# Kernel tuning notes

Measured on AMD Instinct MI355X. Metric: run time of the kernel, lower is better.

Reference implementation:

```python
import jax, jax.numpy as jnp
import numpy as np

POINT_SAMPLE_NUM = 4096
CHAMFER_W = 1.0
NORM_W = 0.1
EDGE_W = 0.5
EPS = 1e-12


def _face_geometry(vertices, faces):
    # vertices: [B, V, 3], faces: [F, 3] int -> per-face verts, areas, unit normals
    v0 = vertices[:, faces[:, 0]]  # [B, F, 3]
    v1 = vertices[:, faces[:, 1]]
    v2 = vertices[:, faces[:, 2]]
    cross = jnp.cross(v1 - v0, v2 - v0)            # [B, F, 3]
    area2 = jnp.linalg.norm(cross, axis=-1)        # [B, F] (= 2*area)
    normals = cross / (area2[..., None] + EPS)     # unit face normals
    return v0, v1, v2, 0.5 * area2, normals


def _sample_points(vertices, faces, n_samples, key):
    # area-weighted face sampling + uniform barycentric coords
    B = vertices.shape[0]
    v0, v1, v2, area, normals = _face_geometry(vertices, faces)
    k_face, k_u, k_v = jax.random.split(key, 3)
    logits = jnp.log(area + EPS)                   # [B, F]
    face_idx = jax.random.categorical(k_face, logits[:, None, :], axis=-1,
                                      shape=(B, n_samples))  # [B, N]
    gather = lambda a: jnp.take_along_axis(a, face_idx[..., None], axis=1)
    p0, p1, p2 = gather(v0), gather(v1), gather(v2)           # [B, N, 3]
    u = jax.random.uniform(k_u, (B, n_samples, 1))
    v = jax.random.uniform(k_v, (B, n_samples, 1))
    r1 = jnp.sqrt(u)
    points = (1.0 - r1) * p0 + r1 * (1.0 - v) * p1 + r1 * v * p2  # [B, N, 3]
    point_normals = gather(normals)                                # [B, N, 3]
    return points, point_normals


def _chamfer(x, y):
    # x: [B, N, 3], y: [B, M, 3] -> squared-distance chamfer + nn indices
    x2 = jnp.sum(x * x, axis=-1)                   # [B, N]
    y2 = jnp.sum(y * y, axis=-1)                   # [B, M]
    d2 = x2[:, :, None] + y2[:, None, :] - 2.0 * jnp.einsum('bnd,bmd->bnm', x, y)
    d2 = jnp.maximum(d2, 0.0)
    idx_x2y = jnp.argmin(d2, axis=2)               # [B, N] nearest y for each x
    min_x2y = jnp.min(d2, axis=2)
    min_y2x = jnp.min(d2, axis=1)
    return jnp.mean(min_x2y) + jnp.mean(min_y2x), idx_x2y


def _edge_loss(vertices, faces):
    v0 = vertices[:, faces[:, 0]]
    v1 = vertices[:, faces[:, 1]]
    v2 = vertices[:, faces[:, 2]]
    e = jnp.concatenate([v1 - v0, v2 - v1, v0 - v2], axis=1)  # [B, 3F, 3]
    return jnp.mean(jnp.sum(e * e, axis=-1))


def setup_inputs() -> dict:
    key = jax.random.key(0)
    k1, k2, k3, k4 = jax.random.split(key, 4)
    predicted_vertices = jax.random.normal(k1, (4, 2562, 3), dtype=jnp.float32)
    predicted_faces = jax.random.randint(k2, (5120, 3), 0, 2562, dtype=jnp.int64)
    gt_vertices = jax.random.normal(k3, (4, 6890, 3), dtype=jnp.float32)
    gt_faces = jax.random.randint(k4, (13776, 3), 0, 6890, dtype=jnp.int64)
    return {"predicted_vertices": predicted_vertices,
            "predicted_faces": predicted_faces,
            "gt_vertices": gt_vertices,
            "gt_faces": gt_faces}


def reference(predicted_vertices, predicted_faces, gt_vertices, gt_faces):
    key = jax.random.key(42)
    kp, kg = jax.random.split(key)
    pred_pts, pred_nrm = _sample_points(predicted_vertices, predicted_faces,
                                        POINT_SAMPLE_NUM, kp)
    gt_pts, gt_nrm = _sample_points(gt_vertices, gt_faces, POINT_SAMPLE_NUM, kg)
    chamfer, idx_p2g = _chamfer(pred_pts, gt_pts)
    # normal consistency between each predicted point and its nearest gt point
    matched_gt_nrm = jnp.take_along_axis(gt_nrm, idx_p2g[..., None], axis=1)
    cos = jnp.abs(jnp.sum(pred_nrm * matched_gt_nrm, axis=-1))  # [B, N]
    normal_loss = jnp.mean(1.0 - cos)
    edge_loss = _edge_loss(predicted_vertices, predicted_faces)
    return CHAMFER_W * chamfer + NORM_W * normal_loss + EDGE_W * edge_loss
```

## Files before the change

kernel.cpp:

```cpp
#include <hip/hip_runtime.h>
#include <stdint.h>

constexpr int   kB  = 4;
constexpr int   kNS = 4096;
constexpr int   kVP = 2562;
constexpr int   kFP = 5120;
constexpr int   kVG = 6890;
constexpr int   kFG = 13776;
constexpr float kEPS  = 1e-12f;
constexpr int   kPB  = 256;
constexpr int   kPREP_P = (kB * kFP + 255) / 256;
constexpr int   kPREP_G = (kB * kFG + 255) / 256;

__host__ __device__ inline void tf2x32(uint32_t k0, uint32_t k1,
                                       uint32_t& x0r, uint32_t& x1r) {
  uint32_t ks2 = k0 ^ k1 ^ 0x1BD11BDAu;
  uint32_t x0 = x0r + k0, x1 = x1r + k1;
#define TF_R(r) { x0 += x1; x1 = (x1 << (r)) | (x1 >> (32 - (r))); x1 ^= x0; }
  TF_R(13) TF_R(15) TF_R(26) TF_R(6)
  x0 += k1;  x1 += ks2 + 1u;
  TF_R(17) TF_R(29) TF_R(16) TF_R(24)
  x0 += ks2; x1 += k0 + 2u;
  TF_R(13) TF_R(15) TF_R(26) TF_R(6)
  x0 += k0;  x1 += k1 + 3u;
  TF_R(17) TF_R(29) TF_R(16) TF_R(24)
  x0 += k1;  x1 += ks2 + 4u;
  TF_R(13) TF_R(15) TF_R(26) TF_R(6)
  x0 += ks2; x1 += k0 + 5u;
#undef TF_R
  x0r = x0; x1r = x1;
}

__device__ inline float bits_to_unit(uint32_t b) {
  return __uint_as_float((b >> 9) | 0x3f800000u) - 1.0f;
}

__device__ inline int faces_is64(const int* __restrict__ faces) {
  return (faces[1] == 0 && faces[3] == 0 && faces[5] == 0 && faces[7] == 0) ? 1 : 0;
}
__device__ inline int face_vtx(const int* __restrict__ faces, int f, int c,
                               int is64, int V) {
  int e = f * 3 + c;
  int v = faces[is64 ? (e << 1) : e];
  return v < 0 ? 0 : (v >= V ? V - 1 : v);
}

__global__ void mlk_write_scalar(float* out, float val) {
  if (threadIdx.x == 0 && blockIdx.x == 0) out[0] = val;
}

__global__ __launch_bounds__(256) void mlk_prep_faces2(
    const float* __restrict__ pverts, const int* __restrict__ pfaces,
    const float* __restrict__ gverts, const int* __restrict__ gfaces,
    float* __restrict__ wp, float* __restrict__ np,
    float* __restrict__ wg, float* __restrict__ ng) {
  int which = blockIdx.x >= kPREP_P;
  int blk   = which ? blockIdx.x - kPREP_P : blockIdx.x;
  const float* verts = which ? gverts : pverts;
  const int*   faces = which ? gfaces : pfaces;
  float* warea = which ? wg : wp;
  float* fnrm  = which ? ng : np;
  int V = which ? kVG : kVP;
  int F = which ? kFG : kFP;
  int idx = blk * 256 + threadIdx.x;
  if (idx >= kB * F) return;
  int is64 = faces_is64(faces);
  int b = idx / F, f = idx - b * F;
  int i0 = face_vtx(faces, f, 0, is64, V);
  int i1 = face_vtx(faces, f, 1, is64, V);
  int i2 = face_vtx(faces, f, 2, is64, V);
  const float* vb = verts + (size_t)b * V * 3;
  float ax = vb[i0*3+0], ay = vb[i0*3+1], az = vb[i0*3+2];
  float bx = vb[i1*3+0], by = vb[i1*3+1], bz = vb[i1*3+2];
  float cx = vb[i2*3+0], cy = vb[i2*3+1], cz = vb[i2*3+2];
  float e1x = bx-ax, e1y = by-ay, e1z = bz-az;
  float e2x = cx-ax, e2y = cy-ay, e2z = cz-az;
  float nx = e1y*e2z - e1z*e2y;
  float ny = e1z*e2x - e1x*e2z;
  float nz = e1x*e2y - e1y*e2x;
  float area2 = sqrtf(nx*nx + ny*ny + nz*nz);
  warea[idx] = 0.5f * area2 + kEPS;
  float inv_n = 1.0f / (area2 + kEPS);
  fnrm[3*idx+0] = nx*inv_n;
  fnrm[3*idx+1] = ny*inv_n;
  fnrm[3*idx+2] = nz*inv_n;
}

__global__ __launch_bounds__(256) void mlk_prefix2(
    float* __restrict__ wp, float* __restrict__ wg) {
  int which = blockIdx.x >> 2;
  int b = blockIdx.x & 3, tid = threadIdx.x;
  int F = which ? kFG : kFP;
  float* wb = (which ? wg : wp) + (size_t)b * F;
  int C = (F + 255) / 256;
  int lo = tid * C;
  int hi = lo + C; if (hi > F) hi = F; if (lo > F) lo = F;
  float s = 0.f;
  for (int i = lo; i < hi; ++i) s += wb[i];
  __shared__ float ps[256];
  ps[tid] = s;
  __syncthreads();
  for (int off = 1; off < 256; off <<= 1) {
    float v = (tid >= off) ? ps[tid - off] : 0.f;
    __syncthreads();
    ps[tid] += v;
    __syncthreads();
  }
  float p = ps[tid] - s;
  for (int i = lo; i < hi; ++i) { p += wb[i]; wb[i] = p; }
}

__global__ __launch_bounds__(256) void mlk_sample_gen(
    const float* __restrict__ pverts, const int* __restrict__ pfaces,
    const float* __restrict__ pref_p, const float* __restrict__ fnrm_p,
    float* __restrict__ pred_pts, float* __restrict__ pred_nrm,
    const float* __restrict__ gverts, const int* __restrict__ gfaces,
    const float* __restrict__ pref_g, const float* __restrict__ fnrm_g,
    float* __restrict__ gt_pts, float* __restrict__ gt_nrm,
    uint32_t pf0, uint32_t pf1, uint32_t pu0, uint32_t pu1, uint32_t pv0, uint32_t pv1,
    uint32_t gf0, uint32_t gf1, uint32_t gu0, uint32_t gu1, uint32_t gv0, uint32_t gv1) {
  int which = blockIdx.x >> 5;
  int t = ((blockIdx.x & 31) << 8) + threadIdx.x;
  const float* verts = which ? gverts : pverts;
  const int*   faces = which ? gfaces : pfaces;
  const float* pref  = which ? pref_g : pref_p;
  const float* fnrm  = which ? fnrm_g : fnrm_p;
  float* pts  = which ? gt_pts : pred_pts;
  float* pnrm = which ? gt_nrm : pred_nrm;
  int V = which ? kVG : kVP;
  int F = which ? kFG : kFP;
  uint32_t kf0 = which ? gf0 : pf0, kf1 = which ? gf1 : pf1;
  uint32_t ku0 = which ? gu0 : pu0, ku1 = which ? gu1 : pu1;
  uint32_t kv0 = which ? gv0 : pv0, kv1 = which ? gv1 : pv1;
  int is64 = faces_is64(faces);

  uint32_t fx0 = (uint32_t)t, fx1 = (uint32_t)(t + 8192);
  tf2x32(kf0, kf1, fx0, fx1);
  uint32_t ux0 = (uint32_t)t, ux1 = (uint32_t)(t + 8192);
  tf2x32(ku0, ku1, ux0, ux1);
  uint32_t vx0 = (uint32_t)t, vx1 = (uint32_t)(t + 8192);
  tf2x32(kv0, kv1, vx0, vx1);

#pragma unroll
  for (int half = 0; half < 2; ++half) {
    int i = t + half * 8192;
    int b = i >> 12;
    float uf = bits_to_unit(half ? fx1 : fx0);
    const float* Pb = pref + (size_t)b * F;
    float target = uf * Pb[F - 1];
    int lo = 0, hi = F - 1;
    while (lo < hi) {
      int mid = (lo + hi) >> 1;
      if (Pb[mid] > target) hi = mid; else lo = mid + 1;
    }
    int fid = lo;
    float u = bits_to_unit(half ? ux1 : ux0);
    float v = bits_to_unit(half ? vx1 : vx0);
    const float* vb = verts + (size_t)b * V * 3;
    int i0 = face_vtx(faces, fid, 0, is64, V);
    int i1 = face_vtx(faces, fid, 1, is64, V);
    int i2 = face_vtx(faces, fid, 2, is64, V);
    float r1 = sqrtf(u);
    float w0 = 1.0f - r1, w1 = r1 * (1.0f - v), w2 = r1 * v;
#pragma unroll
    for (int c = 0; c < 3; ++c) {
      pts[i*3+c] = w0 * vb[i0*3+c] + w1 * vb[i1*3+c] + w2 * vb[i2*3+c];
      pnrm[i*3+c] = fnrm[((size_t)b*F + fid)*3 + c];
    }
  }
}

__global__ __launch_bounds__(256) void mlk_chamfer2(
    const float* __restrict__ pred_pts, const float* __restrict__ gt_pts,
    float* __restrict__ min_p2g, float* __restrict__ min_g2p,
    int* __restrict__ idx_p2g) {
  int bid = blockIdx.x;
  int dir = bid >> 8;
  int r   = bid & 255;
  int b   = r >> 6;
  int qc  = r & 63;
  const float* qpts = dir ? gt_pts   : pred_pts;
  const float* rpts = dir ? pred_pts : gt_pts;
  int wave = threadIdx.x >> 6;
  int lane = threadIdx.x & 63;

  __shared__ float4 lpx4[kNS/4], lpy4[kNS/4], lpz4[kNS/4];
  float* lpx = (float*)lpx4; float* lpy = (float*)lpy4; float* lpz = (float*)lpz4;
  const float* rb = rpts + (size_t)b * kNS * 3;
  for (int i = threadIdx.x; i < kNS; i += 256) {
    lpx[i] = rb[3*i+0];
    lpy[i] = rb[3*i+1];
    lpz[i] = rb[3*i+2];
  }
  __syncthreads();

  int q  = qc * 64 + lane;
  int gi = b * kNS + q;
  float px = qpts[gi*3+0], py = qpts[gi*3+1], pz = qpts[gi*3+2];
  int j0 = wave * (kNS/4/4) * 4;
  j0 = wave * 256;
  float best; int bidx = 0;

  if (dir == 0) {
    float bA = INFINITY, bB = INFINITY; int iA = 0, iB = 0;
#pragma unroll 2
    for (int j = j0; j < j0 + 256; ++j) {
      float4 X = lpx4[j], Y = lpy4[j], Z = lpz4[j];
      int m = j << 2;
      float dx, dy, dz;
      dx = px-X.x; dy = py-Y.x; dz = pz-Z.x; float d0 = dx*dx+dy*dy+dz*dz;
      dx = px-X.y; dy = py-Y.y; dz = pz-Z.y; float d1 = dx*dx+dy*dy+dz*dz;
      dx = px-X.z; dy = py-Y.z; dz = pz-Z.z; float d2 = dx*dx+dy*dy+dz*dz;
      dx = px-X.w; dy = py-Y.w; dz = pz-Z.w; float d3 = dx*dx+dy*dy+dz*dz;
      if (d0 < bA) { bA = d0; iA = m; }
      if (d1 < bA) { bA = d1; iA = m | 1; }
      if (d2 < bB) { bB = d2; iB = m | 2; }
      if (d3 < bB) { bB = d3; iB = m | 3; }
    }
    if (bB < bA || (bB == bA && iB < iA)) { best = bB; bidx = iB; }
    else                                  { best = bA; bidx = iA; }
  } else {
    float bA = INFINITY, bB = INFINITY;
#pragma unroll 2
    for (int j = j0; j < j0 + 256; ++j) {
      float4 X = lpx4[j], Y = lpy4[j], Z = lpz4[j];
      float dx, dy, dz;
      dx = px-X.x; dy = py-Y.x; dz = pz-Z.x; float d0 = dx*dx+dy*dy+dz*dz;
      dx = px-X.y; dy = py-Y.y; dz = pz-Z.y; float d1 = dx*dx+dy*dy+dz*dz;
      dx = px-X.z; dy = py-Y.z; dz = pz-Z.z; float d2 = dx*dx+dy*dy+dz*dz;
      dx = px-X.w; dy = py-Y.w; dz = pz-Z.w; float d3 = dx*dx+dy*dy+dz*dz;
      bA = fminf(bA, fminf(d0, d1));
      bB = fminf(bB, fminf(d2, d3));
    }
    best = fminf(bA, bB);
  }

  __shared__ float cv[4][64];
  __shared__ int   ci[4][64];
  cv[wave][lane] = best; ci[wave][lane] = bidx;
  __syncthreads();
  if (wave == 0) {
    float bv = cv[0][lane]; int bi = ci[0][lane];
#pragma unroll
    for (int wv = 1; wv < 4; ++wv) {
      float v = cv[wv][lane];
      int   i = ci[wv][lane];
      if (v < bv || (v == bv && i < bi)) { bv = v; bi = i; }
    }
    if (dir == 0) { min_p2g[gi] = bv; idx_p2g[gi] = bi; }
    else          { min_g2p[gi] = bv; }
  }
}

__global__ __launch_bounds__(256) void mlk_loss_partial(
    const float* __restrict__ min_p2g, const float* __restrict__ min_g2p,
    const float* __restrict__ pred_nrm, const float* __restrict__ gt_nrm,
    const int* __restrict__ idx_p2g,
    const float* __restrict__ pverts, const int* __restrict__ pfaces,
    float* __restrict__ partial) {
  int tid = threadIdx.x;
  int gidx = blockIdx.x * 256 + tid;
  const int stride = kPB * 256;
  int is64 = faces_is64(pfaces);
  float s1 = 0.f, s2 = 0.f, sc = 0.f, se = 0.f;
  for (int i = gidx; i < kB * kNS; i += stride) {
    s1 += min_p2g[i];
    s2 += min_g2p[i];
    int b = i >> 12;
    int m = idx_p2g[i];
    m = m < 0 ? 0 : (m >= kNS ? kNS - 1 : m);
    const float* pn = pred_nrm + (size_t)i * 3;
    const float* gn = gt_nrm + ((size_t)b * kNS + m) * 3;
    sc += fabsf(pn[0]*gn[0] + pn[1]*gn[1] + pn[2]*gn[2]);
  }
  for (int e = gidx; e < kB * kFP * 3; e += stride) {
    int b = e / (kFP * 3);
    int r = e - b * kFP * 3;
    int f = r / 3, k = r - f * 3;
    int ia, ib;
    if (k == 0)      { ia = face_vtx(pfaces, f, 0, is64, kVP); ib = face_vtx(pfaces, f, 1, is64, kVP); }
    else if (k == 1) { ia = face_vtx(pfaces, f, 1, is64, kVP); ib = face_vtx(pfaces, f, 2, is64, kVP); }
    else             { ia = face_vtx(pfaces, f, 2, is64, kVP); ib = face_vtx(pfaces, f, 0, is64, kVP); }
    const float* vb = pverts + (size_t)b * kVP * 3;
    float dx = vb[ib*3+0] - vb[ia*3+0];
    float dy = vb[ib*3+1] - vb[ia*3+1];
    float dz = vb[ib*3+2] - vb[ia*3+2];
    se += dx*dx + dy*dy + dz*dz;
  }
  __shared__ float r1a[256], r2a[256], r3a[256], r4a[256];
  r1a[tid] = s1; r2a[tid] = s2; r3a[tid] = sc; r4a[tid] = se;
  __syncthreads();
  for (int off = 128; off > 0; off >>= 1) {
    if (tid < off) {
      r1a[tid] += r1a[tid+off];
      r2a[tid] += r2a[tid+off];
      r3a[tid] += r3a[tid+off];
      r4a[tid] += r4a[tid+off];
    }
    __syncthreads();
  }
  if (tid == 0) {
    partial[blockIdx.x*4+0] = r1a[0];
    partial[blockIdx.x*4+1] = r2a[0];
    partial[blockIdx.x*4+2] = r3a[0];
    partial[blockIdx.x*4+3] = r4a[0];
  }
}

__global__ __launch_bounds__(256) void mlk_loss_combine(
    const float* __restrict__ partial, float* __restrict__ out) {
  int tid = threadIdx.x;
  __shared__ float r1a[256], r2a[256], r3a[256], r4a[256];
  r1a[tid] = partial[tid*4+0];
  r2a[tid] = partial[tid*4+1];
  r3a[tid] = partial[tid*4+2];
  r4a[tid] = partial[tid*4+3];
  __syncthreads();
  for (int off = 128; off > 0; off >>= 1) {
    if (tid < off) {
      r1a[tid] += r1a[tid+off];
      r2a[tid] += r2a[tid+off];
      r3a[tid] += r3a[tid+off];
      r4a[tid] += r4a[tid+off];
    }
    __syncthreads();
  }
  if (tid == 0) {
    const float invN = 1.0f / (float)(kB * kNS);
    float chamfer = r1a[0] * invN + r2a[0] * invN;
    float nloss = 1.0f - r3a[0] * invN;
    float eloss = r4a[0] / (float)(kB * kFP * 3);
    out[0] = 1.0f * chamfer + 0.1f * nloss + 0.5f * eloss;
  }
}

extern "C" void kernel_launch(void* const* d_in, const int* in_sizes, int n_in,
                              void* d_out, int out_size, void* d_ws, size_t ws_size,
                              hipStream_t stream) {
  const float* pverts = (const float*)d_in[0];
  const int*   pfaces = (const int*)d_in[1];
  const float* gverts = (const float*)d_in[2];
  const int*   gfaces = (const int*)d_in[3];
  float* out = (float*)d_out;

  const size_t needF =
      (size_t)kB*kFP + (size_t)kB*kFG +
      (size_t)kB*kFP*3 + (size_t)kB*kFG*3 +
      4*(size_t)kB*kNS*3 +
      2*(size_t)kB*kNS +
      (size_t)kPB*4 +
      (size_t)kB*kNS;
  if (ws_size < needF * 4) {
    mlk_write_scalar<<<1, 64, 0, stream>>>(out, -1.0f);
    return;
  }

  uint32_t a0 = 0u, a1 = 2u; tf2x32(0u, 42u, a0, a1);
  uint32_t b0 = 1u, b1 = 3u; tf2x32(0u, 42u, b0, b1);
  uint32_t kp0 = a0, kp1 = b0;
  uint32_t kg0 = a1, kg1 = b1;
  uint32_t kpred[6], kgt[6];
  {
    uint32_t p0 = 0u, p1 = 3u; tf2x32(kp0, kp1, p0, p1);
    uint32_t q0 = 1u, q1 = 4u; tf2x32(kp0, kp1, q0, q1);
    uint32_t r0 = 2u, r1 = 5u; tf2x32(kp0, kp1, r0, r1);
    kpred[0]=p0; kpred[1]=q0; kpred[2]=r0; kpred[3]=p1; kpred[4]=q1; kpred[5]=r1;
  }
  {
    uint32_t p0 = 0u, p1 = 3u; tf2x32(kg0, kg1, p0, p1);
    uint32_t q0 = 1u, q1 = 4u; tf2x32(kg0, kg1, q0, q1);
    uint32_t r0 = 2u, r1 = 5u; tf2x32(kg0, kg1, r0, r1);
    kgt[0]=p0; kgt[1]=q0; kgt[2]=r0; kgt[3]=p1; kgt[4]=q1; kgt[5]=r1;
  }

  float* ws = (float*)d_ws;
  float* pref_p   = ws; ws += kB * kFP;
  float* pref_g   = ws; ws += kB * kFG;
  float* fnrm_p   = ws; ws += kB * kFP * 3;
  float* fnrm_g   = ws; ws += kB * kFG * 3;
  float* pred_pts = ws; ws += kB * kNS * 3;
  float* gt_pts   = ws; ws += kB * kNS * 3;
  float* pred_nrm = ws; ws += kB * kNS * 3;
  float* gt_nrm   = ws; ws += kB * kNS * 3;
  float* min_p2g  = ws; ws += kB * kNS;
  float* min_g2p  = ws; ws += kB * kNS;
  float* partial  = ws; ws += kPB * 4;
  int* idx_p2g = (int*)ws; ws += kB * kNS;

  mlk_prep_faces2<<<kPREP_P + kPREP_G, 256, 0, stream>>>(
      pverts, pfaces, gverts, gfaces, pref_p, fnrm_p, pref_g, fnrm_g);

  mlk_prefix2<<<8, 256, 0, stream>>>(pref_p, pref_g);

  mlk_sample_gen<<<64, 256, 0, stream>>>(
      pverts, pfaces, pref_p, fnrm_p, pred_pts, pred_nrm,
      gverts, gfaces, pref_g, fnrm_g, gt_pts, gt_nrm,
      kpred[0], kpred[1], kpred[2], kpred[3], kpred[4], kpred[5],
      kgt[0],  kgt[1],  kgt[2],  kgt[3],  kgt[4],  kgt[5]);

  mlk_chamfer2<<<512, 256, 0, stream>>>(pred_pts, gt_pts, min_p2g, min_g2p, idx_p2g);

  mlk_loss_partial<<<kPB, 256, 0, stream>>>(min_p2g, min_g2p, pred_nrm, gt_nrm, idx_p2g,
                                            pverts, pfaces, partial);
  mlk_loss_combine<<<1, 256, 0, stream>>>(partial, out);
}
```

Measured before the change: 81.12 us.

## Fuse final reduction via atomic ticket, register-block chamfer, interleave binary searches

The final combine kernel is folded into the partial-loss kernel. The last block to finish, picked by an atomic ticket counter that the prep kernel resets, does the final reduction. This removes one launch. The chamfer kernel now uses 512-thread blocks where each thread handles two query points, so every shared-memory load of reference points is reused twice. Sample generation runs as smaller 64-thread blocks with the two binary searches interleaved to overlap their memory latency. This adds atomic and fence overhead and raises register pressure in the chamfer loop.

```diff
diff --git a/kernel.cpp b/kernel.cpp
--- a/kernel.cpp
+++ b/kernel.cpp
@@ -53,7 +53,9 @@
     const float* __restrict__ pverts, const int* __restrict__ pfaces,
     const float* __restrict__ gverts, const int* __restrict__ gfaces,
     float* __restrict__ wp, float* __restrict__ np,
-    float* __restrict__ wg, float* __restrict__ ng) {
+    float* __restrict__ wg, float* __restrict__ ng,
+    unsigned int* __restrict__ counter) {
+  if (blockIdx.x == 0 && threadIdx.x == 0) *counter = 0u;
   int which = blockIdx.x >= kPREP_P;
   int blk   = which ? blockIdx.x - kPREP_P : blockIdx.x;
   const float* verts = which ? gverts : pverts;
@@ -110,7 +112,7 @@
   for (int i = lo; i < hi; ++i) { p += wb[i]; wb[i] = p; }
 }
 
-__global__ __launch_bounds__(256) void mlk_sample_gen(
+__global__ __launch_bounds__(64) void mlk_sample_gen(
     const float* __restrict__ pverts, const int* __restrict__ pfaces,
     const float* __restrict__ pref_p, const float* __restrict__ fnrm_p,
     float* __restrict__ pred_pts, float* __restrict__ pred_nrm,
@@ -119,8 +121,9 @@
     float* __restrict__ gt_pts, float* __restrict__ gt_nrm,
     uint32_t pf0, uint32_t pf1, uint32_t pu0, uint32_t pu1, uint32_t pv0, uint32_t pv1,
     uint32_t gf0, uint32_t gf1, uint32_t gu0, uint32_t gu1, uint32_t gv0, uint32_t gv1) {
-  int which = blockIdx.x >> 5;
-  int t = ((blockIdx.x & 31) << 8) + threadIdx.x;
+  int g = blockIdx.x * 64 + threadIdx.x;
+  int which = g >> 13;
+  int t = g & 8191;
   const float* verts = which ? gverts : pverts;
   const int*   faces = which ? gfaces : pfaces;
   const float* pref  = which ? pref_g : pref_p;
@@ -141,19 +144,29 @@
   uint32_t vx0 = (uint32_t)t, vx1 = (uint32_t)(t + 8192);
   tf2x32(kv0, kv1, vx0, vx1);
 
+  int b0 = t >> 12, b1 = b0 + 2;
+  const float* P0 = pref + (size_t)b0 * F;
+  const float* P1 = pref + (size_t)b1 * F;
+  float tg0 = bits_to_unit(fx0) * P0[F - 1];
+  float tg1 = bits_to_unit(fx1) * P1[F - 1];
+  int lo0 = 0, hi0 = F - 1, lo1 = 0, hi1 = F - 1;
+  while (lo0 < hi0 || lo1 < hi1) {
+    if (lo0 < hi0) {
+      int mid = (lo0 + hi0) >> 1;
+      if (P0[mid] > tg0) hi0 = mid; else lo0 = mid + 1;
+    }
+    if (lo1 < hi1) {
+      int mid = (lo1 + hi1) >> 1;
+      if (P1[mid] > tg1) hi1 = mid; else lo1 = mid + 1;
+    }
+  }
+  int fid0 = lo0, fid1 = lo1;
+
 #pragma unroll
   for (int half = 0; half < 2; ++half) {
     int i = t + half * 8192;
     int b = i >> 12;
-    float uf = bits_to_unit(half ? fx1 : fx0);
-    const float* Pb = pref + (size_t)b * F;
-    float target = uf * Pb[F - 1];
-    int lo = 0, hi = F - 1;
-    while (lo < hi) {
-      int mid = (lo + hi) >> 1;
-      if (Pb[mid] > target) hi = mid; else lo = mid + 1;
-    }
-    int fid = lo;
+    int fid = half ? fid1 : fid0;
     float u = bits_to_unit(half ? ux1 : ux0);
     float v = bits_to_unit(half ? vx1 : vx0);
     const float* vb = verts + (size_t)b * V * 3;
@@ -170,15 +183,15 @@
   }
 }
 
-__global__ __launch_bounds__(256) void mlk_chamfer2(
+__global__ __launch_bounds__(512) void mlk_chamfer3(
     const float* __restrict__ pred_pts, const float* __restrict__ gt_pts,
     float* __restrict__ min_p2g, float* __restrict__ min_g2p,
     int* __restrict__ idx_p2g) {
   int bid = blockIdx.x;
-  int dir = bid >> 8;
-  int r   = bid & 255;
-  int b   = r >> 6;
-  int qc  = r & 63;
+  int dir = bid >> 7;
+  int r   = bid & 127;
+  int b   = r >> 5;
+  int qc  = r & 31;
   const float* qpts = dir ? gt_pts   : pred_pts;
   const float* rpts = dir ? pred_pts : gt_pts;
   int wave = threadIdx.x >> 6;
@@ -187,77 +200,90 @@
   __shared__ float4 lpx4[kNS/4], lpy4[kNS/4], lpz4[kNS/4];
   float* lpx = (float*)lpx4; float* lpy = (float*)lpy4; float* lpz = (float*)lpz4;
   const float* rb = rpts + (size_t)b * kNS * 3;
-  for (int i = threadIdx.x; i < kNS; i += 256) {
+  for (int i = threadIdx.x; i < kNS; i += 512) {
     lpx[i] = rb[3*i+0];
     lpy[i] = rb[3*i+1];
     lpz[i] = rb[3*i+2];
   }
   __syncthreads();
 
-  int q  = qc * 64 + lane;
-  int gi = b * kNS + q;
-  float px = qpts[gi*3+0], py = qpts[gi*3+1], pz = qpts[gi*3+2];
-  int j0 = wave * (kNS/4/4) * 4;
-  j0 = wave * 256;
-  float best; int bidx = 0;
+  int q0 = qc * 128 + lane;
+  int gq0 = b * kNS + q0;
+  int gq1 = gq0 + 64;
+  float px0 = qpts[gq0*3+0], py0 = qpts[gq0*3+1], pz0 = qpts[gq0*3+2];
+  float px1 = qpts[gq1*3+0], py1 = qpts[gq1*3+1], pz1 = qpts[gq1*3+2];
+  int j0 = wave * 128;
+  float best0, best1; int bidx0 = 0, bidx1 = 0;
 
   if (dir == 0) {
-    float bA = INFINITY, bB = INFINITY; int iA = 0, iB = 0;
+    float bA0 = INFINITY, bB0 = INFINITY, bA1 = INFINITY, bB1 = INFINITY;
+    int iA0 = 0, iB0 = 0, iA1 = 0, iB1 = 0;
 #pragma unroll 2
-    for (int j = j0; j < j0 + 256; ++j) {
+    for (int j = j0; j < j0 + 128; ++j) {
       float4 X = lpx4[j], Y = lpy4[j], Z = lpz4[j];
       int m = j << 2;
-      float dx, dy, dz;
-      dx = px-X.x; dy = py-Y.x; dz = pz-Z.x; float d0 = dx*dx+dy*dy+dz*dz;
-      dx = px-X.y; dy = py-Y.y; dz = pz-Z.y; float d1 = dx*dx+dy*dy+dz*dz;
-      dx = px-X.z; dy = py-Y.z; dz = pz-Z.z; float d2 = dx*dx+dy*dy+dz*dz;
-      dx = px-X.w; dy = py-Y.w; dz = pz-Z.w; float d3 = dx*dx+dy*dy+dz*dz;
-      if (d0 < bA) { bA = d0; iA = m; }
-      if (d1 < bA) { bA = d1; iA = m | 1; }
-      if (d2 < bB) { bB = d2; iB = m | 2; }
-      if (d3 < bB) { bB = d3; iB = m | 3; }
-    }
-    if (bB < bA || (bB == bA && iB < iA)) { best = bB; bidx = iB; }
-    else                                  { best = bA; bidx = iA; }
+      float dx, dy, dz, d;
+      dx = px0-X.x; dy = py0-Y.x; dz = pz0-Z.x; d = dx*dx+dy*dy+dz*dz; if (d < bA0) { bA0 = d; iA0 = m; }
+      dx = px0-X.y; dy = py0-Y.y; dz = pz0-Z.y; d = dx*dx+dy*dy+dz*dz; if (d < bA0) { bA0 = d; iA0 = m|1; }
+      dx = px0-X.z; dy = py0-Y.z; dz = pz0-Z.z; d = dx*dx+dy*dy+dz*dz; if (d < bB0) { bB0 = d; iB0 = m|2; }
+      dx = px0-X.w; dy = py0-Y.w; dz = pz0-Z.w; d = dx*dx+dy*dy+dz*dz; if (d < bB0) { bB0 = d; iB0 = m|3; }
+      dx = px1-X.x; dy = py1-Y.x; dz = pz1-Z.x; d = dx*dx+dy*dy+dz*dz; if (d < bA1) { bA1 = d; iA1 = m; }
+      dx = px1-X.y; dy = py1-Y.y; dz = pz1-Z.y; d = dx*dx+dy*dy+dz*dz; if (d < bA1) { bA1 = d; iA1 = m|1; }
+      dx = px1-X.z; dy = py1-Y.z; dz = pz1-Z.z; d = dx*dx+dy*dy+dz*dz; if (d < bB1) { bB1 = d; iB1 = m|2; }
+      dx = px1-X.w; dy = py1-Y.w; dz = pz1-Z.w; d = dx*dx+dy*dy+dz*dz; if (d < bB1) { bB1 = d; iB1 = m|3; }
+    }
+    if (bB0 < bA0 || (bB0 == bA0 && iB0 < iA0)) { best0 = bB0; bidx0 = iB0; } else { best0 = bA0; bidx0 = iA0; }
+    if (bB1 < bA1 || (bB1 == bA1 && iB1 < iA1)) { best1 = bB1; bidx1 = iB1; } else { best1 = bA1; bidx1 = iA1; }
   } else {
-    float bA = INFINITY, bB = INFINITY;
+    float bA0 = INFINITY, bB0 = INFINITY, bA1 = INFINITY, bB1 = INFINITY;
 #pragma unroll 2
-    for (int j = j0; j < j0 + 256; ++j) {
+    for (int j = j0; j < j0 + 128; ++j) {
       float4 X = lpx4[j], Y = lpy4[j], Z = lpz4[j];
       float dx, dy, dz;
-      dx = px-X.x; dy = py-Y.x; dz = pz-Z.x; float d0 = dx*dx+dy*dy+dz*dz;
-      dx = px-X.y; dy = py-Y.y; dz = pz-Z.y; float d1 = dx*dx+dy*dy+dz*dz;
-      dx = px-X.z; dy = py-Y.z; dz = pz-Z.z; float d2 = dx*dx+dy*dy+dz*dz;
-      dx = px-X.w; dy = py-Y.w; dz = pz-Z.w; float d3 = dx*dx+dy*dy+dz*dz;
-      bA = fminf(bA, fminf(d0, d1));
-      bB = fminf(bB, fminf(d2, d3));
-    }
-    best = fminf(bA, bB);
-  }
-
-  __shared__ float cv[4][64];
-  __shared__ int   ci[4][64];
-  cv[wave][lane] = best; ci[wave][lane] = bidx;
+      dx = px0-X.x; dy = py0-Y.x; dz = pz0-Z.x; float d0 = dx*dx+dy*dy+dz*dz;
+      dx = px0-X.y; dy = py0-Y.y; dz = pz0-Z.y; float d1 = dx*dx+dy*dy+dz*dz;
+      dx = px0-X.z; dy = py0-Y.z; dz = pz0-Z.z; float d2 = dx*dx+dy*dy+dz*dz;
+      dx = px0-X.w; dy = py0-Y.w; dz = pz0-Z.w; float d3 = dx*dx+dy*dy+dz*dz;
+      bA0 = fminf(bA0, fminf(d0, d1));
+      bB0 = fminf(bB0, fminf(d2, d3));
+      dx = px1-X.x; dy = py1-Y.x; dz = pz1-Z.x; d0 = dx*dx+dy*dy+dz*dz;
+      dx = px1-X.y; dy = py1-Y.y; dz = pz1-Z.y; d1 = dx*dx+dy*dy+dz*dz;
+      dx = px1-X.z; dy = py1-Y.z; dz = pz1-Z.z; d2 = dx*dx+dy*dy+dz*dz;
+      dx = px1-X.w; dy = py1-Y.w; dz = pz1-Z.w; d3 = dx*dx+dy*dy+dz*dz;
+      bA1 = fminf(bA1, fminf(d0, d1));
+      bB1 = fminf(bB1, fminf(d2, d3));
+    }
+    best0 = fminf(bA0, bB0);
+    best1 = fminf(bA1, bB1);
+  }
+
+  __shared__ float cv[8][128];
+  __shared__ int   ci[8][128];
+  cv[wave][lane]      = best0; ci[wave][lane]      = bidx0;
+  cv[wave][lane + 64] = best1; ci[wave][lane + 64] = bidx1;
   __syncthreads();
-  if (wave == 0) {
-    float bv = cv[0][lane]; int bi = ci[0][lane];
+  if (threadIdx.x < 128) {
+    int ql = threadIdx.x;
+    float bv = cv[0][ql]; int bi = ci[0][ql];
 #pragma unroll
-    for (int wv = 1; wv < 4; ++wv) {
-      float v = cv[wv][lane];
-      int   i = ci[wv][lane];
+    for (int wv = 1; wv < 8; ++wv) {
+      float v = cv[wv][ql];
+      int   i = ci[wv][ql];
       if (v < bv || (v == bv && i < bi)) { bv = v; bi = i; }
     }
+    int gi = b * kNS + qc * 128 + ql;
     if (dir == 0) { min_p2g[gi] = bv; idx_p2g[gi] = bi; }
     else          { min_g2p[gi] = bv; }
   }
 }
 
-__global__ __launch_bounds__(256) void mlk_loss_partial(
+__global__ __launch_bounds__(256) void mlk_loss(
     const float* __restrict__ min_p2g, const float* __restrict__ min_g2p,
     const float* __restrict__ pred_nrm, const float* __restrict__ gt_nrm,
     const int* __restrict__ idx_p2g,
     const float* __restrict__ pverts, const int* __restrict__ pfaces,
-    float* __restrict__ partial) {
+    float* __restrict__ partial, unsigned int* __restrict__ counter,
+    float* __restrict__ out) {
   int tid = threadIdx.x;
   int gidx = blockIdx.x * 256 + tid;
   const int stride = kPB * 256;
@@ -305,32 +331,34 @@
     partial[blockIdx.x*4+2] = r3a[0];
     partial[blockIdx.x*4+3] = r4a[0];
   }
-}
-
-__global__ __launch_bounds__(256) void mlk_loss_combine(
-    const float* __restrict__ partial, float* __restrict__ out) {
-  int tid = threadIdx.x;
-  __shared__ float r1a[256], r2a[256], r3a[256], r4a[256];
-  r1a[tid] = partial[tid*4+0];
-  r2a[tid] = partial[tid*4+1];
-  r3a[tid] = partial[tid*4+2];
-  r4a[tid] = partial[tid*4+3];
+  __threadfence();
+  __shared__ unsigned int ticket;
+  if (tid == 0) ticket = atomicAdd(counter, 1u);
   __syncthreads();
-  for (int off = 128; off > 0; off >>= 1) {
-    if (tid < off) {
-      r1a[tid] += r1a[tid+off];
-      r2a[tid] += r2a[tid+off];
-      r3a[tid] += r3a[tid+off];
-      r4a[tid] += r4a[tid+off];
-    }
+  if (ticket == kPB - 1) {
+    __threadfence();
+    volatile const float* vp = partial;
+    r1a[tid] = vp[tid*4+0];
+    r2a[tid] = vp[tid*4+1];
+    r3a[tid] = vp[tid*4+2];
+    r4a[tid] = vp[tid*4+3];
     __syncthreads();
-  }
-  if (tid == 0) {
-    const float invN = 1.0f / (float)(kB * kNS);
-    float chamfer = r1a[0] * invN + r2a[0] * invN;
-    float nloss = 1.0f - r3a[0] * invN;
-    float eloss = r4a[0] / (float)(kB * kFP * 3);
-    out[0] = 1.0f * chamfer + 0.1f * nloss + 0.5f * eloss;
+    for (int off = 128; off > 0; off >>= 1) {
+      if (tid < off) {
+        r1a[tid] += r1a[tid+off];
+        r2a[tid] += r2a[tid+off];
+        r3a[tid] += r3a[tid+off];
+        r4a[tid] += r4a[tid+off];
+      }
+      __syncthreads();
+    }
+    if (tid == 0) {
+      const float invN = 1.0f / (float)(kB * kNS);
+      float chamfer = r1a[0] * invN + r2a[0] * invN;
+      float nloss = 1.0f - r3a[0] * invN;
+      float eloss = r4a[0] / (float)(kB * kFP * 3);
+      out[0] = 1.0f * chamfer + 0.1f * nloss + 0.5f * eloss;
+    }
   }
 }
 
@@ -348,7 +376,7 @@
       (size_t)kB*kFP*3 + (size_t)kB*kFG*3 +
       4*(size_t)kB*kNS*3 +
       2*(size_t)kB*kNS +
-      (size_t)kPB*4 +
+      (size_t)kPB*4 + 1 +
       (size_t)kB*kNS;
   if (ws_size < needF * 4) {
     mlk_write_scalar<<<1, 64, 0, stream>>>(out, -1.0f);
@@ -385,22 +413,22 @@
   float* min_p2g  = ws; ws += kB * kNS;
   float* min_g2p  = ws; ws += kB * kNS;
   float* partial  = ws; ws += kPB * 4;
+  unsigned int* counter = (unsigned int*)ws; ws += 1;
   int* idx_p2g = (int*)ws; ws += kB * kNS;
 
   mlk_prep_faces2<<<kPREP_P + kPREP_G, 256, 0, stream>>>(
-      pverts, pfaces, gverts, gfaces, pref_p, fnrm_p, pref_g, fnrm_g);
+      pverts, pfaces, gverts, gfaces, pref_p, fnrm_p, pref_g, fnrm_g, counter);
 
   mlk_prefix2<<<8, 256, 0, stream>>>(pref_p, pref_g);
 
-  mlk_sample_gen<<<64, 256, 0, stream>>>(
+  mlk_sample_gen<<<256, 64, 0, stream>>>(
       pverts, pfaces, pref_p, fnrm_p, pred_pts, pred_nrm,
       gverts, gfaces, pref_g, fnrm_g, gt_pts, gt_nrm,
       kpred[0], kpred[1], kpred[2], kpred[3], kpred[4], kpred[5],
       kgt[0],  kgt[1],  kgt[2],  kgt[3],  kgt[4],  kgt[5]);
 
-  mlk_chamfer2<<<512, 256, 0, stream>>>(pred_pts, gt_pts, min_p2g, min_g2p, idx_p2g);
-
-  mlk_loss_partial<<<kPB, 256, 0, stream>>>(min_p2g, min_g2p, pred_nrm, gt_nrm, idx_p2g,
-                                            pverts, pfaces, partial);
-  mlk_loss_combine<<<1, 256, 0, stream>>>(partial, out);
-}
+  mlk_chamfer3<<<256, 512, 0, stream>>>(pred_pts, gt_pts, min_p2g, min_g2p, idx_p2g);
+
+  mlk_loss<<<kPB, 256, 0, stream>>>(min_p2g, min_g2p, pred_nrm, gt_nrm, idx_p2g,
+                                    pverts, pfaces, partial, counter, out);
+}
```

New measurement: 100.3 us. +23.7%, slower.
